# Optimization experiments

Measured on AMD Instinct MI355X. Metric: run time of the kernel, lower is better.

## Reference

```python
import jax, jax.numpy as jnp
import numpy as np

# init config (from init_kwargs)
NUM_ANCHORS = 5
NUM_CLASSES = 80
ANCHORS = jnp.array([[0.57273, 0.677385], [1.87446, 2.06253], [3.33843, 5.47434],
                     [7.88282, 3.52778], [9.77052, 9.16828]], dtype=jnp.float32)
MAX_BOXES = 50  # hard-coded loop bound in build_targets


def setup_inputs() -> dict:
    key = jax.random.key(0)
    k1, k2 = jax.random.split(key)
    output = jax.random.normal(k1, (64, 425, 38, 38), dtype=jnp.float32)
    # target: (nB, 50*5) of [cls, cx, cy, w, h] normalized to (0,1); strictly
    # positive entries -> all 50 boxes valid (original loop breaks at first 0).
    target = jax.random.uniform(k2, (64, 250), dtype=jnp.float32, minval=0.02, maxval=0.98)
    return {"output": output, "target": target, "reqd_class_index": 14}


def _cls_mask(target, nH, nW):
    """Vectorized build_targets: only cls_mask affects the returned loss.
    For each valid GT box, best anchor = argmax IoU of (0,0,aw,ah) vs (0,0,gw,gh)
    (first max wins, matching the strict > in the Python loop); mark cell
    (b, best_n, gj, gi)."""
    nB = target.shape[0]
    tgt = target.reshape(nB, MAX_BOXES, 5)
    # loop breaks at first t with target[b][5t+1]==0 -> cumulative validity
    valid = jnp.cumprod((tgt[:, :, 1] != 0).astype(jnp.int32), axis=1) > 0
    gx = tgt[:, :, 1] * nW
    gy = tgt[:, :, 2] * nH
    gw = tgt[:, :, 3] * nW  # (nB, T)
    gh = tgt[:, :, 4] * nH
    gi = jnp.clip(jnp.floor(gx).astype(jnp.int32), 0, nW - 1)
    gj = jnp.clip(jnp.floor(gy).astype(jnp.int32), 0, nH - 1)
    aw, ah = ANCHORS[:, 0], ANCHORS[:, 1]  # (nA,)
    # centered-box IoU: intersection widths are min of the widths
    inter = jnp.minimum(gw[..., None], aw) * jnp.minimum(gh[..., None], ah)  # (nB,T,nA)
    iou = inter / (gw[..., None] * gh[..., None] + aw * ah - inter)
    best_n = jnp.argmax(iou, axis=-1).astype(jnp.int32)  # (nB, T), first-max tiebreak
    b = jnp.arange(nB, dtype=jnp.int32)[:, None]
    flat = ((b * NUM_ANCHORS + best_n) * nH + gj) * nW + gi  # (nB, T)
    n_cells = nB * NUM_ANCHORS * nH * nW
    mask = jnp.zeros((n_cells,), jnp.int32).at[flat.ravel()].max(valid.ravel().astype(jnp.int32))
    return mask > 0


def reference(output, target, reqd_class_index):
    nB, _, nH, nW = output.shape
    out = output.reshape(nB, NUM_ANCHORS, 5 + NUM_CLASSES, nH, nW)
    # class logits -> (nB, nA, nH, nW, nC), matching torch's
    # view(nB*nA, nC, nH*nW).transpose(1,2).view(-1, nC) flattening order
    cls_logits = jnp.transpose(out[:, :, 5:, :, :], (0, 1, 3, 4, 2))
    probs = jax.nn.softmax(cls_logits, axis=-1)
    p = probs[..., reqd_class_index].reshape(-1)  # prob of required class per cell
    mask = _cls_mask(target, nH, nW)
    m = mask.astype(p.dtype)
    # L1Loss(cls_prob2, 0, size_average=True) over selected cells == masked mean
    loss = jnp.sum(p * m) / jnp.sum(m)
    max_class_prob = jnp.max(jnp.where(mask, p, -jnp.inf))
    return loss, max_class_prob
```

## Files before the change

### kernel.cpp

```cpp
#include <hip/hip_runtime.h>
#include <stdint.h>
#include <math.h>

#define NUM_ANCHORS 5
#define NUM_CLASSES 80
#define MAX_BOXES   50


__global__ void init_ws(uint32_t* ws, int n_words) {
    int i = blockIdx.x * blockDim.x + threadIdx.x;
    if (i < n_words) ws[i] = (i == 2) ? 0xFF800000u : 0u;
}

__global__ void build_list(const float* __restrict__ target,
                           uint32_t* __restrict__ hdr,
                           int* __restrict__ list,
                           uint32_t* __restrict__ bm,
                           int nH, int nW) {
#pragma clang fp contract(off)
    int b = blockIdx.x;
    int lane = threadIdx.x;
    const float* t = target + (long)b * MAX_BOXES * 5;
    float x = 1.0f, y = 0.0f, w = 0.0f, h = 0.0f;
    if (lane < MAX_BOXES) {
        x = t[lane * 5 + 1];
        y = t[lane * 5 + 2];
        w = t[lane * 5 + 3];
        h = t[lane * 5 + 4];
    }
    unsigned long long zb = __ballot(lane < MAX_BOXES && x == 0.0f);
    int first_zero = zb ? (__ffsll(zb) - 1) : MAX_BOXES;
    if (lane >= first_zero) return;

    float gx = x * (float)nW;
    float gy = y * (float)nH;
    float gw = w * (float)nW;
    float gh = h * (float)nH;
    int gi = min(max((int)floorf(gx), 0), nW - 1);
    int gj = min(max((int)floorf(gy), 0), nH - 1);

    const float aw[NUM_ANCHORS] = {0.57273f, 1.87446f, 3.33843f, 7.88282f, 9.77052f};
    const float ah[NUM_ANCHORS] = {0.677385f, 2.06253f, 5.47434f, 3.52778f, 9.16828f};
    int best = 0; float bestiou = -1.0f;
    #pragma unroll
    for (int n = 0; n < NUM_ANCHORS; ++n) {
        float inter = fminf(gw, aw[n]) * fminf(gh, ah[n]);
        float uni   = gw * gh + aw[n] * ah[n] - inter;
        float iou   = inter / uni;
        if (iou > bestiou) { bestiou = iou; best = n; }
    }
    int flat = ((b * NUM_ANCHORS + best) * nH + gj) * nW + gi;
    uint32_t bit = 1u << (flat & 31);
    uint32_t old = atomicOr(&bm[flat >> 5], bit);
    if (!(old & bit)) {
        int idx = (int)atomicAdd(&hdr[1], 1u);
        list[idx] = flat;
    }
}

__global__ void __launch_bounds__(256)
reduce_list(const float* __restrict__ output,
            const uint32_t* __restrict__ hdr,
            const int* __restrict__ list,
            float* __restrict__ sumf,
            int* __restrict__ maxbits,
            const int* __restrict__ reqd,
            int HW) {
    __shared__ float sp[4];
    __shared__ float sm[4];
    int lane = threadIdx.x & 63;
    int wave = threadIdx.x >> 6;
    int g = blockIdx.x * 4 + wave;
    int count = (int)hdr[1];
    float p = 0.0f, pm = -INFINITY;
    if (g < count) {
        int cell = list[g];
        int ba = cell / HW;
        int hw = cell - ba * HW;
        const float* ptr = output + ((long)(ba * (5 + NUM_CLASSES) + 5)) * HW + hw;
        float v0 = ptr[(long)lane * HW];
        float v1 = (lane < NUM_CLASSES - 64) ? ptr[(long)(lane + 64) * HW] : -INFINITY;
        float mx = fmaxf(v0, v1);
        #pragma unroll
        for (int off = 32; off; off >>= 1) mx = fmaxf(mx, __shfl_xor(mx, off, 64));
        float e0 = expf(v0 - mx);
        float e1 = (lane < NUM_CLASSES - 64) ? expf(v1 - mx) : 0.0f;
        float s = e0 + e1;
        #pragma unroll
        for (int off = 32; off; off >>= 1) s += __shfl_xor(s, off, 64);
        int rq = *reqd;
        float lr = (rq < 64) ? __shfl(v0, rq, 64) : __shfl(v1, rq - 64, 64);
        p = expf(lr - mx) / s;
        pm = p;
    }
    if (lane == 0) { sp[wave] = p; sm[wave] = pm; }
    __syncthreads();
    if (threadIdx.x == 0) {
        float ts = 0.0f, tm = -INFINITY;
        #pragma unroll
        for (int w = 0; w < 4; ++w) { ts += sp[w]; tm = fmaxf(tm, sm[w]); }
        if (tm > -INFINITY) {
            atomicAdd(sumf, ts);
            atomicMax(maxbits, __float_as_int(tm));
        }
    }
}

__global__ void finalize(const float* __restrict__ sumf,
                         const uint32_t* __restrict__ hdr,
                         const int* __restrict__ maxbits,
                         float* __restrict__ out) {
    out[0] = sumf[0] / (float)hdr[1];
    out[1] = __int_as_float(maxbits[0]);
}

extern "C" void kernel_launch(void* const* d_in, const int* in_sizes, int n_in,
                              void* d_out, int out_size, void* d_ws, size_t ws_size,
                              hipStream_t stream) {
    const float* output = (const float*)d_in[0];
    const float* target = (const float*)d_in[1];
    const int*   reqd   = (const int*)d_in[2];
    float* out = (float*)d_out;

    int nB = in_sizes[1] / (MAX_BOXES * 5);
    int HW = in_sizes[0] / (nB * (5 + NUM_CLASSES) * NUM_ANCHORS);
    int nW = 1; while (nW * nW < HW) ++nW;
    int nH = HW / nW;
    long cells = (long)nB * NUM_ANCHORS * nH * nW;

    int listCap = nB * MAX_BOXES;
    int bmWords = (int)((cells + 31) / 32);
    int n_words = 4 + listCap + bmWords;

    uint32_t* ws   = (uint32_t*)d_ws;
    uint32_t* hdr  = ws;
    float*    sumf = (float*)ws;
    int*      maxb = (int*)(ws + 2);
    int*      list = (int*)(ws + 4);
    uint32_t* bm   = ws + 4 + listCap;

    init_ws<<<(n_words + 255) / 256, 256, 0, stream>>>(ws, n_words);

    build_list<<<nB, 64, 0, stream>>>(target, hdr, list, bm, nH, nW);

    int rblocks = (listCap + 3) / 4;
    reduce_list<<<rblocks, 256, 0, stream>>>(output, hdr, list, sumf, maxb,
                                             reqd, HW);

    finalize<<<1, 1, 0, stream>>>(sumf, hdr, maxb, out);
}
```

Baseline: 213.8 us.

## Dedupe cells in-wave, drop bitmap init, fuse finalize via last-block ticket

Per-batch duplicate cells are now found with a wave shuffle scan instead of a global bitmap and atomicOr. Each batch writes a compacted list and its own count, so the large bitmap no longer has to be zeroed and init shrinks to a single small block. The finalize kernel is folded into the reduction through a threadfence plus last-block ticket, which removes one launch. The cost is a 50-step shuffle loop per wave and a serial sum over nB counts in the last block.

```diff
diff --git a/kernel.cpp b/kernel.cpp
--- a/kernel.cpp
+++ b/kernel.cpp
@@ -8,14 +8,13 @@
 
 
 __global__ void init_ws(uint32_t* ws, int n_words) {
-    int i = blockIdx.x * blockDim.x + threadIdx.x;
+    int i = threadIdx.x;
     if (i < n_words) ws[i] = (i == 2) ? 0xFF800000u : 0u;
 }
 
 __global__ void build_list(const float* __restrict__ target,
-                           uint32_t* __restrict__ hdr,
+                           uint32_t* __restrict__ cnt,
                            int* __restrict__ list,
-                           uint32_t* __restrict__ bm,
                            int nH, int nW) {
 #pragma clang fp contract(off)
     int b = blockIdx.x;
@@ -30,50 +29,62 @@
     }
     unsigned long long zb = __ballot(lane < MAX_BOXES && x == 0.0f);
     int first_zero = zb ? (__ffsll(zb) - 1) : MAX_BOXES;
-    if (lane >= first_zero) return;
+    bool valid = (lane < MAX_BOXES) && (lane < first_zero);
 
-    float gx = x * (float)nW;
-    float gy = y * (float)nH;
-    float gw = w * (float)nW;
-    float gh = h * (float)nH;
-    int gi = min(max((int)floorf(gx), 0), nW - 1);
-    int gj = min(max((int)floorf(gy), 0), nH - 1);
-
-    const float aw[NUM_ANCHORS] = {0.57273f, 1.87446f, 3.33843f, 7.88282f, 9.77052f};
-    const float ah[NUM_ANCHORS] = {0.677385f, 2.06253f, 5.47434f, 3.52778f, 9.16828f};
-    int best = 0; float bestiou = -1.0f;
+    int flat = -1 - lane;
+    if (valid) {
+        float gx = x * (float)nW;
+        float gy = y * (float)nH;
+        float gw = w * (float)nW;
+        float gh = h * (float)nH;
+        int gi = min(max((int)floorf(gx), 0), nW - 1);
+        int gj = min(max((int)floorf(gy), 0), nH - 1);
+        const float aw[NUM_ANCHORS] = {0.57273f, 1.87446f, 3.33843f, 7.88282f, 9.77052f};
+        const float ah[NUM_ANCHORS] = {0.677385f, 2.06253f, 5.47434f, 3.52778f, 9.16828f};
+        int best = 0; float bestiou = -1.0f;
+        #pragma unroll
+        for (int n = 0; n < NUM_ANCHORS; ++n) {
+            float inter = fminf(gw, aw[n]) * fminf(gh, ah[n]);
+            float uni   = gw * gh + aw[n] * ah[n] - inter;
+            float iou   = inter / uni;
+            if (iou > bestiou) { bestiou = iou; best = n; }
+        }
+        flat = ((b * NUM_ANCHORS + best) * nH + gj) * nW + gi;
+    }
+    bool dup = false;
     #pragma unroll
-    for (int n = 0; n < NUM_ANCHORS; ++n) {
-        float inter = fminf(gw, aw[n]) * fminf(gh, ah[n]);
-        float uni   = gw * gh + aw[n] * ah[n] - inter;
-        float iou   = inter / uni;
-        if (iou > bestiou) { bestiou = iou; best = n; }
+    for (int j = 0; j < MAX_BOXES; ++j) {
+        int fj = __shfl(flat, j, 64);
+        if (j < lane && fj == flat) dup = true;
     }
-    int flat = ((b * NUM_ANCHORS + best) * nH + gj) * nW + gi;
-    uint32_t bit = 1u << (flat & 31);
-    uint32_t old = atomicOr(&bm[flat >> 5], bit);
-    if (!(old & bit)) {
-        int idx = (int)atomicAdd(&hdr[1], 1u);
-        list[idx] = flat;
+    bool keep = valid && !dup;
+    unsigned long long kb = __ballot(keep);
+    if (keep) {
+        int rank = __popcll(kb & ((1ull << lane) - 1ull));
+        list[b * MAX_BOXES + rank] = flat;
     }
+    if (lane == 0) cnt[b] = (uint32_t)__popcll(kb);
 }
 
 __global__ void __launch_bounds__(256)
-reduce_list(const float* __restrict__ output,
-            const uint32_t* __restrict__ hdr,
-            const int* __restrict__ list,
-            float* __restrict__ sumf,
-            int* __restrict__ maxbits,
-            const int* __restrict__ reqd,
-            int HW) {
+reduce_fused(const float* __restrict__ output,
+             const uint32_t* __restrict__ cnt,
+             const int* __restrict__ list,
+             float* __restrict__ sumf,
+             int* __restrict__ maxbits,
+             uint32_t* __restrict__ ticket,
+             const int* __restrict__ reqd,
+             float* __restrict__ out,
+             int HW, int nB) {
     __shared__ float sp[4];
     __shared__ float sm[4];
     int lane = threadIdx.x & 63;
     int wave = threadIdx.x >> 6;
     int g = blockIdx.x * 4 + wave;
-    int count = (int)hdr[1];
+    int b = g / MAX_BOXES;
+    int i = g - b * MAX_BOXES;
     float p = 0.0f, pm = -INFINITY;
-    if (g < count) {
+    if (b < nB && i < (int)cnt[b]) {
         int cell = list[g];
         int ba = cell / HW;
         int hw = cell - ba * HW;
@@ -103,15 +114,17 @@
             atomicAdd(sumf, ts);
             atomicMax(maxbits, __float_as_int(tm));
         }
+        __threadfence();
+        uint32_t t = atomicAdd(ticket, 1u);
+        if (t == (uint32_t)(gridDim.x - 1)) {
+            float s  = atomicAdd(sumf, 0.0f);
+            int   mb = atomicMax(maxbits, (int)0x80000000);
+            int total = 0;
+            for (int bb = 0; bb < nB; ++bb) total += (int)cnt[bb];
+            out[0] = s / (float)total;
+            out[1] = __int_as_float(mb);
+        }
     }
-}
-
-__global__ void finalize(const float* __restrict__ sumf,
-                         const uint32_t* __restrict__ hdr,
-                         const int* __restrict__ maxbits,
-                         float* __restrict__ out) {
-    out[0] = sumf[0] / (float)hdr[1];
-    out[1] = __int_as_float(maxbits[0]);
 }
 
 extern "C" void kernel_launch(void* const* d_in, const int* in_sizes, int n_in,
@@ -126,26 +139,21 @@
     int HW = in_sizes[0] / (nB * (5 + NUM_CLASSES) * NUM_ANCHORS);
     int nW = 1; while (nW * nW < HW) ++nW;
     int nH = HW / nW;
-    long cells = (long)nB * NUM_ANCHORS * nH * nW;
-
-    int listCap = nB * MAX_BOXES;
-    int bmWords = (int)((cells + 31) / 32);
-    int n_words = 4 + listCap + bmWords;
 
     uint32_t* ws   = (uint32_t*)d_ws;
-    uint32_t* hdr  = ws;
     float*    sumf = (float*)ws;
+    uint32_t* tick = ws + 1;
     int*      maxb = (int*)(ws + 2);
-    int*      list = (int*)(ws + 4);
-    uint32_t* bm   = ws + 4 + listCap;
+    uint32_t* cnt  = ws + 4;
+    int*      list = (int*)(ws + 4 + nB);
 
-    init_ws<<<(n_words + 255) / 256, 256, 0, stream>>>(ws, n_words);
+    int n_words = 4 + nB;
+    init_ws<<<1, 128, 0, stream>>>(ws, n_words);
 
-    build_list<<<nB, 64, 0, stream>>>(target, hdr, list, bm, nH, nW);
+    build_list<<<nB, 64, 0, stream>>>(target, cnt, list, nH, nW);
 
-    int rblocks = (listCap + 3) / 4;
-    reduce_list<<<rblocks, 256, 0, stream>>>(output, hdr, list, sumf, maxb,
-                                             reqd, HW);
-
-    finalize<<<1, 1, 0, stream>>>(sumf, hdr, maxb, out);
+    int slots = nB * MAX_BOXES;
+    int rblocks = (slots + 3) / 4;
+    reduce_fused<<<rblocks, 256, 0, stream>>>(output, cnt, list, sumf, maxb,
+                                              tick, reqd, out, HW, nB);
 }
```

Result: slower. 227.4 us (+6.4%).
